# Kernel tuning notes

Measured on AMD Instinct MI355X. Metric: run time of the kernel, lower is better.

The kernel has to match this reference:

```python
import jax, jax.numpy as jnp
import numpy as np
from jax import lax

B, CIN, COUT, H, W, K = 256, 512, 256, 8, 8, 8192


def setup_inputs() -> dict:
    key = jax.random.key(0)
    ks = jax.random.split(key, 6)
    scale = 0.05
    return {
        "latent": jax.random.normal(ks[0], (B, CIN, H, W), dtype=jnp.float32),
        "conv_w": jax.random.normal(ks[1], (COUT, CIN, 3, 3), dtype=jnp.float32) * scale,
        "conv_b": jax.random.normal(ks[2], (COUT,), dtype=jnp.float32) * scale,
        "lin_w": jax.random.normal(ks[3], (COUT, COUT), dtype=jnp.float32) * scale,
        "lin_b": jax.random.normal(ks[4], (COUT,), dtype=jnp.float32) * scale,
        "emb": jax.random.normal(ks[5], (K, COUT), dtype=jnp.float32),
    }


def reference(latent, conv_w, conv_b, lin_w, lin_b, emb):
    # pre-quantization conv: 3x3, stride 1, padding 1 (SAME), NCHW / OIHW
    x = lax.conv_general_dilated(
        latent, conv_w, window_strides=(1, 1), padding="SAME",
        dimension_numbers=("NCHW", "OIHW", "NCHW"),
    ) + conv_b[None, :, None, None]
    # permute(0,2,3,1) then linear on last dim
    x = jnp.transpose(x, (0, 2, 3, 1))              # [B,H,W,C]
    x = jnp.einsum("bhwc,dc->bhwd", x, lin_w) + lin_b
    flat = x.reshape(-1, x.shape[-1])               # [B*H*W, C]
    distances = (
        jnp.sum(flat ** 2, axis=1, keepdims=True)
        + jnp.sum(emb ** 2, axis=1)
        - 2.0 * flat @ emb.T
    )                                               # [B*H*W, K]
    encoding_indices = jnp.argmin(distances, axis=1)
    return encoding_indices.reshape(-1, 64)
```

## Files before the change

kernel.cpp:

```cpp
#include <hip/hip_runtime.h>
#include <cstdint>
#include <cstddef>


#define CIN_  512
#define E_    4608
#define M_    16384

typedef _Float16 half4_t __attribute__((ext_vector_type(4)));
typedef _Float16 half8_t __attribute__((ext_vector_type(8)));
typedef float f32x4 __attribute__((ext_vector_type(4)));

#define GLOAD_LDS16(gptr, lptr)                                         \
    __builtin_amdgcn_global_load_lds(                                   \
        (const __attribute__((address_space(1))) unsigned int*)(gptr),  \
        (__attribute__((address_space(3))) unsigned int*)(lptr), 16, 0, 0)

__global__ void tkern(const float* __restrict__ src, float* __restrict__ dst,
                      int R, int C) {
    __shared__ float t[32][33];
    int c = blockIdx.x * 32 + threadIdx.x;
    int r = blockIdx.y * 32 + threadIdx.y;
    if (r < R && c < C) t[threadIdx.y][threadIdx.x] = src[(size_t)r * C + c];
    __syncthreads();
    int rr = blockIdx.x * 32 + threadIdx.y;
    int cc = blockIdx.y * 32 + threadIdx.x;
    if (rr < C && cc < R) dst[(size_t)rr * R + cc] = t[threadIdx.x][threadIdx.y];
}

__global__ __launch_bounds__(256) void fold5_k(const float* __restrict__ conv_w,
                                               const float* __restrict__ lwT,
                                               _Float16* __restrict__ W2x) {
    int e0 = blockIdx.x * 8;
    int d = threadIdx.x;
    float acc[8];
    #pragma unroll
    for (int j = 0; j < 8; ++j) acc[j] = 0.f;
    for (int co = 0; co < 256; ++co) {
        float lw = lwT[co * 256 + d];
        const float* cwr = conv_w + (size_t)co * E_ + e0;
        #pragma unroll
        for (int j = 0; j < 8; ++j) acc[j] += cwr[j] * lw;
    }
    #pragma unroll
    for (int j = 0; j < 8; ++j) {
        int e = e0 + j;
        int c = e / 9, t9 = e - c * 9;
        _Float16 h = (_Float16)acc[j];
        _Float16 l = (_Float16)(acc[j] - (float)h);
        W2x[((size_t)(t9 * 256 + d)) * 512 + c] = h;
        W2x[((size_t)((9 + t9) * 256 + d)) * 512 + c] = l;
    }
}

__global__ void bias_k(const float* __restrict__ lwT, const float* __restrict__ conv_b,
                       const float* __restrict__ lin_b, float* __restrict__ b2) {
    int d = threadIdx.x;
    float acc = lin_b[d];
    for (int co = 0; co < 256; ++co) acc += lwT[co * 256 + d] * conv_b[co];
    b2[d] = acc;
}

__global__ void embsq2_k(const float* __restrict__ emb, float* __restrict__ esq) {
    int w = threadIdx.x >> 6, lane = threadIdx.x & 63;
    #pragma unroll
    for (int it = 0; it < 4; ++it) {
        int k = (blockIdx.x + it * 512) * 4 + w;
        const float* row = emb + (size_t)k * 256;
        float s = 0.f;
        #pragma unroll
        for (int i = 0; i < 4; ++i) { float v = row[lane + 64 * i]; s += v * v; }
        #pragma unroll
        for (int m = 32; m >= 1; m >>= 1) s += __shfl_xor(s, m, 64);
        if (lane == 0) esq[k] = s;
    }
}

__global__ __launch_bounds__(256) void packlat_k(const float* __restrict__ lat,
                                                 _Float16* __restrict__ Xnp) {
    int b = blockIdx.x, t = threadIdx.x;
    __shared__ float lt[128][65];
    const float* src = lat + (size_t)b * 512 * 64;
    _Float16* dst = Xnp + (size_t)b * 64 * 1024;
    for (int c0 = 0; c0 < 512; c0 += 128) {
        __syncthreads();
        #pragma unroll
        for (int j = 0; j < 8; ++j) {
            int f4 = t + j * 256;
            int cc = f4 >> 4, p4 = (f4 & 15) * 4;
            float4 v = *(const float4*)(src + (size_t)(c0 + cc) * 64 + p4);
            lt[cc][p4] = v.x; lt[cc][p4 + 1] = v.y;
            lt[cc][p4 + 2] = v.z; lt[cc][p4 + 3] = v.w;
        }
        __syncthreads();
        int pix = t >> 2, cr = (t & 3) * 32;
        #pragma unroll
        for (int q = 0; q < 4; ++q) {
            half8_t hh, ll;
            #pragma unroll
            for (int j = 0; j < 8; ++j) {
                float v = lt[cr + q * 8 + j][pix];
                _Float16 h = (_Float16)v;
                hh[j] = h; ll[j] = (_Float16)(v - (float)h);
            }
            *(half8_t*)(dst + (size_t)pix * 1024 + c0 + cr + q * 8) = hh;
            *(half8_t*)(dst + (size_t)pix * 1024 + 512 + c0 + cr + q * 8) = ll;
        }
    }
}

__global__ __launch_bounds__(256) void convm4_k(
    const _Float16* __restrict__ Xnp, const _Float16* __restrict__ W2x,
    const float* __restrict__ b2, const _Float16* __restrict__ zp,
    float* __restrict__ yb) {
    __shared__ char sm[65536];
    int m0 = blockIdx.x * 128, n0 = blockIdx.y * 128;
    int tid = threadIdx.x, w = tid >> 6, lane = tid & 63;
    int wm = w & 1, wn = w >> 1;
    int fr = lane & 15, fq = lane >> 4;

    int xq = (fq ^ ((fr >> 1) & 3)) << 4;
    int aoff[4], boff[4];
    #pragma unroll
    for (int i = 0; i < 4; ++i) {
        aoff[i] = (wm * 64 + i * 16 + fr) * 64 + xq;
        boff[i] = (wn * 64 + i * 16 + fr) * 64 + xq;
    }
    int slt[2], sr[2], sq[2];
    #pragma unroll
    for (int i = 0; i < 2; ++i) {
        int s = w * 128 + i * 64 + lane;
        slt[i] = s;
        sr[i] = s >> 2;
        sq[i] = ((s & 3) ^ ((s >> 3) & 3)) * 8;
    }

    f32x4 acc[4][4];
    #pragma unroll
    for (int s = 0; s < 4; ++s)
        #pragma unroll
        for (int t = 0; t < 4; ++t)
            #pragma unroll
            for (int r = 0; r < 4; ++r) acc[s][t][r] = 0.f;

    auto stage = [&](int it, int buf) {
        int tap = it >> 4, cc = it & 15;
        int dy = tap / 3 - 1, dx = tap - (tap / 3) * 3 - 1;
        char* L = sm + buf * 32768;
        #pragma unroll
        for (int i = 0; i < 2; ++i) {
            int choff = cc * 32 + sq[i];
            int gm = m0 + sr[i];
            int img = gm >> 6, pix = gm & 63;
            int ih = (pix >> 3) + dy, iw = (pix & 7) + dx;
            bool v = ((unsigned)ih < 8u) && ((unsigned)iw < 8u);
            const _Float16* a0 = v
                ? Xnp + ((size_t)(img * 64 + ih * 8 + iw)) * 1024 : zp;
            const _Float16* a1 = v ? a0 + 512 : zp;
            GLOAD_LDS16(a0 + choff, L + slt[i] * 16);
            GLOAD_LDS16(a1 + choff, L + 8192 + slt[i] * 16);
            const _Float16* bb =
                W2x + ((size_t)(tap * 256 + n0 + sr[i])) * 512 + choff;
            GLOAD_LDS16(bb, L + 16384 + slt[i] * 16);
            GLOAD_LDS16(bb + (size_t)9 * 256 * 512, L + 24576 + slt[i] * 16);
        }
    };

    stage(0, 0);
    for (int it = 0; it < 144; ++it) {
        __syncthreads();
        if (it + 1 < 144) stage(it + 1, (it + 1) & 1);
        const char* L = sm + (it & 1) * 32768;
        half8_t ah[4], al[4], bh[4], bl[4];
        #pragma unroll
        for (int s = 0; s < 4; ++s) ah[s] = *(const half8_t*)(L + aoff[s]);
        #pragma unroll
        for (int t = 0; t < 4; ++t) bh[t] = *(const half8_t*)(L + 16384 + boff[t]);
        #pragma unroll
        for (int s = 0; s < 4; ++s)
            #pragma unroll
            for (int t = 0; t < 4; ++t)
                acc[s][t] = __builtin_amdgcn_mfma_f32_16x16x32_f16(
                    ah[s], bh[t], acc[s][t], 0, 0, 0);
        #pragma unroll
        for (int t = 0; t < 4; ++t) bl[t] = *(const half8_t*)(L + 24576 + boff[t]);
        #pragma unroll
        for (int s = 0; s < 4; ++s)
            #pragma unroll
            for (int t = 0; t < 4; ++t)
                acc[s][t] = __builtin_amdgcn_mfma_f32_16x16x32_f16(
                    ah[s], bl[t], acc[s][t], 0, 0, 0);
        #pragma unroll
        for (int s = 0; s < 4; ++s) al[s] = *(const half8_t*)(L + 8192 + aoff[s]);
        #pragma unroll
        for (int s = 0; s < 4; ++s)
            #pragma unroll
            for (int t = 0; t < 4; ++t)
                acc[s][t] = __builtin_amdgcn_mfma_f32_16x16x32_f16(
                    al[s], bh[t], acc[s][t], 0, 0, 0);
    }

    float bv[4];
    #pragma unroll
    for (int t = 0; t < 4; ++t) bv[t] = b2[n0 + wn * 64 + t * 16 + fr];
    #pragma unroll
    for (int s = 0; s < 4; ++s)
        #pragma unroll
        for (int r = 0; r < 4; ++r) {
            int m = m0 + wm * 64 + s * 16 + fq * 4 + r;
            #pragma unroll
            for (int t = 0; t < 4; ++t) {
                int d = n0 + wn * 64 + t * 16 + fr;
                yb[(size_t)m * 256 + d] = acc[s][t][r] + bv[t];
            }
        }
}

__global__ void packhi_s(const float* __restrict__ x, _Float16* __restrict__ o,
                         int iters) {
    for (int it = 0; it < iters; ++it) {
        int i = (blockIdx.x + it * 512) * 256 + threadIdx.x;
        float4 v = *(const float4*)(x + (size_t)i * 4);
        half4_t h = {(_Float16)v.x, (_Float16)v.y, (_Float16)v.z, (_Float16)v.w};
        *(half4_t*)(o + (size_t)i * 4) = h;
    }
}

__global__ __launch_bounds__(256) void screen6_k(
    const _Float16* __restrict__ A2, const _Float16* __restrict__ B2,
    const float* __restrict__ esq, float* __restrict__ ps2, int* __restrict__ pi2) {
    __shared__ char sm[32768];
    int m0 = blockIdx.x * 128, n0 = blockIdx.y * 128;
    int tid = threadIdx.x, w = tid >> 6, lane = tid & 63;
    int wm = w & 1, wn = w >> 1;
    int fr = lane & 15, fq = lane >> 4;

    int xq = (fq ^ ((fr >> 1) & 3)) << 4;
    int aoff[4], boff[4];
    #pragma unroll
    for (int i = 0; i < 4; ++i) {
        aoff[i] = (wm * 64 + i * 16 + fr) * 64 + xq;
        boff[i] = (wn * 64 + i * 16 + fr) * 64 + xq;
    }
    int slt[2], sr[2], sq[2];
    #pragma unroll
    for (int i = 0; i < 2; ++i) {
        int s = w * 128 + i * 64 + lane;
        slt[i] = s;
        sr[i] = s >> 2;
        sq[i] = ((s & 3) ^ ((s >> 3) & 3)) * 8;
    }

    auto stage = [&](int kt, int buf) {
        char* L = sm + buf * 16384;
        int ko = kt * 32;
        #pragma unroll
        for (int i = 0; i < 2; ++i) {
            GLOAD_LDS16(A2 + (size_t)(m0 + sr[i]) * 256 + ko + sq[i],
                        L + slt[i] * 16);
            GLOAD_LDS16(B2 + (size_t)(n0 + sr[i]) * 256 + ko + sq[i],
                        L + 8192 + slt[i] * 16);
        }
    };

    f32x4 acc[4][4];
    #pragma unroll
    for (int s = 0; s < 4; ++s)
        #pragma unroll
        for (int t = 0; t < 4; ++t)
            #pragma unroll
            for (int r = 0; r < 4; ++r) acc[s][t][r] = 0.f;

    stage(0, 0);
    for (int kt = 0; kt < 8; ++kt) {
        __syncthreads();
        if (kt + 1 < 8) stage(kt + 1, (kt + 1) & 1);
        const char* L = sm + (kt & 1) * 16384;
        half8_t af[4], bf[4];
        #pragma unroll
        for (int s = 0; s < 4; ++s) af[s] = *(const half8_t*)(L + aoff[s]);
        #pragma unroll
        for (int t = 0; t < 4; ++t) bf[t] = *(const half8_t*)(L + 8192 + boff[t]);
        #pragma unroll
        for (int s = 0; s < 4; ++s)
            #pragma unroll
            for (int t = 0; t < 4; ++t)
                acc[s][t] = __builtin_amdgcn_mfma_f32_16x16x32_f16(
                    af[s], bf[t], acc[s][t], 0, 0, 0);
    }

    float esv[4];
    #pragma unroll
    for (int t = 0; t < 4; ++t) esv[t] = esq[n0 + wn * 64 + t * 16 + fr];
    int colIdx = blockIdx.y * 2 + wn;
    #pragma unroll
    for (int s = 0; s < 4; ++s) {
        #pragma unroll
        for (int r = 0; r < 4; ++r) {
            float best = 3.4e38f; int bidx = 0x7fffffff;
            #pragma unroll
            for (int t = 0; t < 4; ++t) {
                float sc = esv[t] - 2.f * acc[s][t][r];
                int k = n0 + wn * 64 + t * 16 + fr;
                if (sc < best || (sc == best && k < bidx)) { best = sc; bidx = k; }
            }
            #pragma unroll
            for (int msk = 1; msk <= 8; msk <<= 1) {
                float so = __shfl_xor(best, msk, 64);
                int ko2 = __shfl_xor(bidx, msk, 64);
                if (so < best || (so == best && ko2 < bidx)) { best = so; bidx = ko2; }
            }
            if (fr == 0) {
                int m = m0 + wm * 64 + s * 16 + fq * 4 + r;
                ps2[(size_t)m * 128 + colIdx] = best;
                pi2[(size_t)m * 128 + colIdx] = bidx;
            }
        }
    }
}

__global__ __launch_bounds__(256) void refine3_k(
    const float* __restrict__ y, const float* __restrict__ emb,
    const float* __restrict__ esq, const float* __restrict__ ps2,
    const int* __restrict__ pi2, int* __restrict__ out) {
    int lane = threadIdx.x & 63;
    for (int j = 0; j < 8; ++j) {
        int m = blockIdx.x * 32 + j * 4 + (threadIdx.x >> 6);
        float4 yv = *(const float4*)(y + (size_t)m * 256 + lane * 4);
        float sc_[2]; int kc_[2];
        #pragma unroll
        for (int i = 0; i < 2; ++i) {
            sc_[i] = ps2[(size_t)m * 128 + lane * 2 + i];
            kc_[i] = pi2[(size_t)m * 128 + lane * 2 + i];
        }
        float s0 = fminf(sc_[0], sc_[1]);
        #pragma unroll
        for (int msk = 1; msk <= 32; msk <<= 1) s0 = fminf(s0, __shfl_xor(s0, msk, 64));
        float thr = s0 + 0.25f;
        float best = 3.4e38f; int bk = 0x7fffffff;
        for (int c = 0; c < 128; ++c) {
            float scc = __shfl(sc_[c & 1], c >> 1, 64);
            if (scc <= thr) {
                int k = __shfl(kc_[c & 1], c >> 1, 64);
                float4 ev = *(const float4*)(emb + (size_t)k * 256 + lane * 4);
                float d = yv.x * ev.x + yv.y * ev.y + yv.z * ev.z + yv.w * ev.w;
                #pragma unroll
                for (int msk = 1; msk <= 32; msk <<= 1) d += __shfl_xor(d, msk, 64);
                float sx = esq[k] - 2.f * d;
                if (sx < best || (sx == best && k < bk)) { best = sx; bk = k; }
            }
        }
        if (lane == 0) out[m] = bk;
    }
}

extern "C" void kernel_launch(void* const* d_in, const int* in_sizes, int n_in,
                              void* d_out, int out_size, void* d_ws, size_t ws_size,
                              hipStream_t stream) {
    const float* latent = (const float*)d_in[0];
    const float* conv_w = (const float*)d_in[1];
    const float* conv_b = (const float*)d_in[2];
    const float* lin_w  = (const float*)d_in[3];
    const float* lin_b  = (const float*)d_in[4];
    const float* emb    = (const float*)d_in[5];
    int* out = (int*)d_out;

    char* W = (char*)d_ws;
    float*    lwT = (float*)(W + 0);
    float*    b2  = (float*)(W + 262144);
    float*    esq = (float*)(W + 263168);
    float*    yb  = (float*)(W + 295936);
    _Float16* W2x = (_Float16*)(W + 17073152);
    _Float16* zp  = (_Float16*)(W + 21791744);
    _Float16* Xnp = (_Float16*)(W + 21792768);
    _Float16* A2  = (_Float16*)(W + 21792768);
    _Float16* B2  = (_Float16*)(W + 30181376);
    float*    ps2 = (float*)(W + 34375680);
    int*      pi2 = (int*)(W + 42764288);

    dim3 t32(32, 32);
    tkern<<<dim3(8, 8), t32, 0, stream>>>(lin_w, lwT, 256, 256);
    bias_k<<<1, 256, 0, stream>>>(lwT, conv_b, lin_b, b2);
    embsq2_k<<<512, 256, 0, stream>>>(emb, esq);
    fold5_k<<<576, 256, 0, stream>>>(conv_w, lwT, W2x);
    hipMemsetAsync(zp, 0, 1024, stream);
    packlat_k<<<256, 256, 0, stream>>>(latent, Xnp);

    convm4_k<<<dim3(128, 2), 256, 0, stream>>>(Xnp, W2x, b2, zp, yb);

    packhi_s<<<512, 256, 0, stream>>>(yb, A2, 8);
    packhi_s<<<512, 256, 0, stream>>>(emb, B2, 4);
    screen6_k<<<dim3(128, 64), 256, 0, stream>>>(A2, B2, esq, ps2, pi2);
    refine3_k<<<512, 256, 0, stream>>>(yb, emb, esq, ps2, pi2, out);
}
```

Baseline: 505.7 us.

## Reuse A tile across conv taps, fuse pack kernels, XCD-aware screen tile mapping

The conv kernel now loads each 128-pixel channel slice of the latent into LDS once per channel chunk and reuses it across all 9 taps. Each tap's shift is applied through the LDS read address with zeroed fragments at borders, so A-side global traffic drops about ninefold and the zero-pad buffer and memset go away. The two fp16 pack launches and the embedding-norm kernel are merged into one kernel. The screen kernel remaps a 1D grid so that blocks sharing M tiles land on the same XCD, which should improve L2 reuse. The cost is more LDS address arithmetic and selects inside the inner loop.

```diff
diff --git a/kernel.cpp b/kernel.cpp
--- a/kernel.cpp
+++ b/kernel.cpp
@@ -61,21 +61,6 @@
     b2[d] = acc;
 }
 
-__global__ void embsq2_k(const float* __restrict__ emb, float* __restrict__ esq) {
-    int w = threadIdx.x >> 6, lane = threadIdx.x & 63;
-    #pragma unroll
-    for (int it = 0; it < 4; ++it) {
-        int k = (blockIdx.x + it * 512) * 4 + w;
-        const float* row = emb + (size_t)k * 256;
-        float s = 0.f;
-        #pragma unroll
-        for (int i = 0; i < 4; ++i) { float v = row[lane + 64 * i]; s += v * v; }
-        #pragma unroll
-        for (int m = 32; m >= 1; m >>= 1) s += __shfl_xor(s, m, 64);
-        if (lane == 0) esq[k] = s;
-    }
-}
-
 __global__ __launch_bounds__(256) void packlat_k(const float* __restrict__ lat,
                                                  _Float16* __restrict__ Xnp) {
     int b = blockIdx.x, t = threadIdx.x;
@@ -109,10 +94,9 @@
     }
 }
 
-__global__ __launch_bounds__(256) void convm4_k(
+__global__ __launch_bounds__(256) void convm6_k(
     const _Float16* __restrict__ Xnp, const _Float16* __restrict__ W2x,
-    const float* __restrict__ b2, const _Float16* __restrict__ zp,
-    float* __restrict__ yb) {
+    const float* __restrict__ b2, float* __restrict__ yb) {
     __shared__ char sm[65536];
     int m0 = blockIdx.x * 128, n0 = blockIdx.y * 128;
     int tid = threadIdx.x, w = tid >> 6, lane = tid & 63;
@@ -120,11 +104,14 @@
     int fr = lane & 15, fq = lane >> 4;
 
     int xq = (fq ^ ((fr >> 1) & 3)) << 4;
-    int aoff[4], boff[4];
-    #pragma unroll
-    for (int i = 0; i < 4; ++i) {
-        aoff[i] = (wm * 64 + i * 16 + fr) * 64 + xq;
-        boff[i] = (wn * 64 + i * 16 + fr) * 64 + xq;
+    int boff[4];
+    #pragma unroll
+    for (int i = 0; i < 4; ++i) boff[i] = (wn * 64 + i * 16 + fr) * 64 + xq;
+    int imgoff[4], ph[4], pw[4];
+    #pragma unroll
+    for (int s = 0; s < 4; ++s) {
+        int rr = wm * 64 + s * 16 + fr;
+        imgoff[s] = rr & 64; ph[s] = (rr >> 3) & 7; pw[s] = rr & 7;
     }
     int slt[2], sr[2], sq[2];
     #pragma unroll
@@ -135,6 +122,27 @@
         sq[i] = ((s & 3) ^ ((s >> 3) & 3)) * 8;
     }
 
+    auto stageA = [&](int cc, int buf) {
+        char* L = sm + buf * 16384;
+        #pragma unroll
+        for (int i = 0; i < 2; ++i) {
+            const _Float16* base =
+                Xnp + (size_t)(m0 + sr[i]) * 1024 + cc * 32 + sq[i];
+            GLOAD_LDS16(base, L + slt[i] * 16);
+            GLOAD_LDS16(base + 512, L + 8192 + slt[i] * 16);
+        }
+    };
+    auto stageB = [&](int tap, int cc, int buf) {
+        char* L = sm + 32768 + buf * 16384;
+        #pragma unroll
+        for (int i = 0; i < 2; ++i) {
+            const _Float16* bb =
+                W2x + ((size_t)(tap * 256 + n0 + sr[i])) * 512 + cc * 32 + sq[i];
+            GLOAD_LDS16(bb, L + slt[i] * 16);
+            GLOAD_LDS16(bb + (size_t)9 * 256 * 512, L + 8192 + slt[i] * 16);
+        }
+    };
+
     f32x4 acc[4][4];
     #pragma unroll
     for (int s = 0; s < 4; ++s)
@@ -143,61 +151,57 @@
             #pragma unroll
             for (int r = 0; r < 4; ++r) acc[s][t][r] = 0.f;
 
-    auto stage = [&](int it, int buf) {
-        int tap = it >> 4, cc = it & 15;
-        int dy = tap / 3 - 1, dx = tap - (tap / 3) * 3 - 1;
-        char* L = sm + buf * 32768;
-        #pragma unroll
-        for (int i = 0; i < 2; ++i) {
-            int choff = cc * 32 + sq[i];
-            int gm = m0 + sr[i];
-            int img = gm >> 6, pix = gm & 63;
-            int ih = (pix >> 3) + dy, iw = (pix & 7) + dx;
-            bool v = ((unsigned)ih < 8u) && ((unsigned)iw < 8u);
-            const _Float16* a0 = v
-                ? Xnp + ((size_t)(img * 64 + ih * 8 + iw)) * 1024 : zp;
-            const _Float16* a1 = v ? a0 + 512 : zp;
-            GLOAD_LDS16(a0 + choff, L + slt[i] * 16);
-            GLOAD_LDS16(a1 + choff, L + 8192 + slt[i] * 16);
-            const _Float16* bb =
-                W2x + ((size_t)(tap * 256 + n0 + sr[i])) * 512 + choff;
-            GLOAD_LDS16(bb, L + 16384 + slt[i] * 16);
-            GLOAD_LDS16(bb + (size_t)9 * 256 * 512, L + 24576 + slt[i] * 16);
-        }
-    };
-
-    stage(0, 0);
-    for (int it = 0; it < 144; ++it) {
-        __syncthreads();
-        if (it + 1 < 144) stage(it + 1, (it + 1) & 1);
-        const char* L = sm + (it & 1) * 32768;
-        half8_t ah[4], al[4], bh[4], bl[4];
-        #pragma unroll
-        for (int s = 0; s < 4; ++s) ah[s] = *(const half8_t*)(L + aoff[s]);
-        #pragma unroll
-        for (int t = 0; t < 4; ++t) bh[t] = *(const half8_t*)(L + 16384 + boff[t]);
-        #pragma unroll
-        for (int s = 0; s < 4; ++s)
-            #pragma unroll
-            for (int t = 0; t < 4; ++t)
-                acc[s][t] = __builtin_amdgcn_mfma_f32_16x16x32_f16(
-                    ah[s], bh[t], acc[s][t], 0, 0, 0);
-        #pragma unroll
-        for (int t = 0; t < 4; ++t) bl[t] = *(const half8_t*)(L + 24576 + boff[t]);
-        #pragma unroll
-        for (int s = 0; s < 4; ++s)
-            #pragma unroll
-            for (int t = 0; t < 4; ++t)
-                acc[s][t] = __builtin_amdgcn_mfma_f32_16x16x32_f16(
-                    ah[s], bl[t], acc[s][t], 0, 0, 0);
-        #pragma unroll
-        for (int s = 0; s < 4; ++s) al[s] = *(const half8_t*)(L + 8192 + aoff[s]);
-        #pragma unroll
-        for (int s = 0; s < 4; ++s)
-            #pragma unroll
-            for (int t = 0; t < 4; ++t)
-                acc[s][t] = __builtin_amdgcn_mfma_f32_16x16x32_f16(
-                    al[s], bh[t], acc[s][t], 0, 0, 0);
+    stageA(0, 0);
+    stageB(0, 0, 0);
+    const half8_t zfrag = {};
+    int gi = 0;
+    for (int cc = 0; cc < 16; ++cc) {
+        const char* Ab = sm + (cc & 1) * 16384;
+        for (int tap = 0; tap < 9; ++tap, ++gi) {
+            __syncthreads();
+            if (tap < 8) stageB(tap + 1, cc, (gi + 1) & 1);
+            else if (cc < 15) stageB(0, cc + 1, (gi + 1) & 1);
+            if (tap == 7 && cc < 15) stageA(cc + 1, (cc + 1) & 1);
+
+            int dy = tap / 3 - 1, dx = tap - (tap / 3) * 3 - 1;
+            half8_t ah[4], al[4];
+            #pragma unroll
+            for (int s = 0; s < 4; ++s) {
+                int ih = ph[s] + dy, iw = pw[s] + dx;
+                bool v = ((unsigned)ih < 8u) && ((unsigned)iw < 8u);
+                int pp = imgoff[s] + (v ? ih * 8 + iw : 0);
+                int ao = pp * 64 + ((fq ^ ((pp >> 1) & 3)) << 4);
+                half8_t a0 = *(const half8_t*)(Ab + ao);
+                half8_t a1 = *(const half8_t*)(Ab + 8192 + ao);
+                ah[s] = v ? a0 : zfrag;
+                al[s] = v ? a1 : zfrag;
+            }
+            const char* Bb = sm + 32768 + (gi & 1) * 16384;
+            half8_t bh[4], bl[4];
+            #pragma unroll
+            for (int t = 0; t < 4; ++t) {
+                bh[t] = *(const half8_t*)(Bb + boff[t]);
+                bl[t] = *(const half8_t*)(Bb + 8192 + boff[t]);
+            }
+            #pragma unroll
+            for (int s = 0; s < 4; ++s)
+                #pragma unroll
+                for (int t = 0; t < 4; ++t)
+                    acc[s][t] = __builtin_amdgcn_mfma_f32_16x16x32_f16(
+                        ah[s], bh[t], acc[s][t], 0, 0, 0);
+            #pragma unroll
+            for (int s = 0; s < 4; ++s)
+                #pragma unroll
+                for (int t = 0; t < 4; ++t)
+                    acc[s][t] = __builtin_amdgcn_mfma_f32_16x16x32_f16(
+                        ah[s], bl[t], acc[s][t], 0, 0, 0);
+            #pragma unroll
+            for (int s = 0; s < 4; ++s)
+                #pragma unroll
+                for (int t = 0; t < 4; ++t)
+                    acc[s][t] = __builtin_amdgcn_mfma_f32_16x16x32_f16(
+                        al[s], bh[t], acc[s][t], 0, 0, 0);
+        }
     }
 
     float bv[4];
@@ -216,21 +220,40 @@
         }
 }
 
-__global__ void packhi_s(const float* __restrict__ x, _Float16* __restrict__ o,
-                         int iters) {
-    for (int it = 0; it < iters; ++it) {
+__global__ __launch_bounds__(256) void pack2_k(
+    const float* __restrict__ yb, const float* __restrict__ emb,
+    _Float16* __restrict__ A2, _Float16* __restrict__ B2,
+    float* __restrict__ esq) {
+    #pragma unroll
+    for (int it = 0; it < 8; ++it) {
         int i = (blockIdx.x + it * 512) * 256 + threadIdx.x;
-        float4 v = *(const float4*)(x + (size_t)i * 4);
+        float4 v = *(const float4*)(yb + (size_t)i * 4);
         half4_t h = {(_Float16)v.x, (_Float16)v.y, (_Float16)v.z, (_Float16)v.w};
-        *(half4_t*)(o + (size_t)i * 4) = h;
-    }
-}
-
-__global__ __launch_bounds__(256) void screen6_k(
+        *(half4_t*)(A2 + (size_t)i * 4) = h;
+    }
+    int w = threadIdx.x >> 6, lane = threadIdx.x & 63;
+    #pragma unroll
+    for (int j = 0; j < 4; ++j) {
+        int k = blockIdx.x * 16 + w * 4 + j;
+        float4 v = *(const float4*)(emb + (size_t)k * 256 + lane * 4);
+        half4_t h = {(_Float16)v.x, (_Float16)v.y, (_Float16)v.z, (_Float16)v.w};
+        *(half4_t*)(B2 + (size_t)k * 256 + lane * 4) = h;
+        float s = v.x * v.x + v.y * v.y + v.z * v.z + v.w * v.w;
+        #pragma unroll
+        for (int m = 32; m >= 1; m >>= 1) s += __shfl_xor(s, m, 64);
+        if (lane == 0) esq[k] = s;
+    }
+}
+
+__global__ __launch_bounds__(256) void screen7_k(
     const _Float16* __restrict__ A2, const _Float16* __restrict__ B2,
     const float* __restrict__ esq, float* __restrict__ ps2, int* __restrict__ pi2) {
     __shared__ char sm[32768];
-    int m0 = blockIdx.x * 128, n0 = blockIdx.y * 128;
+    int Lb = blockIdx.x;
+    int xcd = Lb & 7, j = Lb >> 3;
+    int mt = xcd * 16 + (j & 15);
+    int nt = j >> 4;
+    int m0 = mt * 128, n0 = nt * 128;
     int tid = threadIdx.x, w = tid >> 6, lane = tid & 63;
     int wm = w & 1, wn = w >> 1;
     int fr = lane & 15, fq = lane >> 4;
@@ -292,7 +315,7 @@
     float esv[4];
     #pragma unroll
     for (int t = 0; t < 4; ++t) esv[t] = esq[n0 + wn * 64 + t * 16 + fr];
-    int colIdx = blockIdx.y * 2 + wn;
+    int colIdx = nt * 2 + wn;
     #pragma unroll
     for (int s = 0; s < 4; ++s) {
         #pragma unroll
@@ -371,7 +394,6 @@
     float*    esq = (float*)(W + 263168);
     float*    yb  = (float*)(W + 295936);
     _Float16* W2x = (_Float16*)(W + 17073152);
-    _Float16* zp  = (_Float16*)(W + 21791744);
     _Float16* Xnp = (_Float16*)(W + 21792768);
     _Float16* A2  = (_Float16*)(W + 21792768);
     _Float16* B2  = (_Float16*)(W + 30181376);
@@ -381,15 +403,12 @@
     dim3 t32(32, 32);
     tkern<<<dim3(8, 8), t32, 0, stream>>>(lin_w, lwT, 256, 256);
     bias_k<<<1, 256, 0, stream>>>(lwT, conv_b, lin_b, b2);
-    embsq2_k<<<512, 256, 0, stream>>>(emb, esq);
     fold5_k<<<576, 256, 0, stream>>>(conv_w, lwT, W2x);
-    hipMemsetAsync(zp, 0, 1024, stream);
     packlat_k<<<256, 256, 0, stream>>>(latent, Xnp);
 
-    convm4_k<<<dim3(128, 2), 256, 0, stream>>>(Xnp, W2x, b2, zp, yb);
-
-    packhi_s<<<512, 256, 0, stream>>>(yb, A2, 8);
-    packhi_s<<<512, 256, 0, stream>>>(emb, B2, 4);
-    screen6_k<<<dim3(128, 64), 256, 0, stream>>>(A2, B2, esq, ps2, pi2);
+    convm6_k<<<dim3(128, 2), 256, 0, stream>>>(Xnp, W2x, b2, yb);
+
+    pack2_k<<<512, 256, 0, stream>>>(yb, emb, A2, B2, esq);
+    screen7_k<<<8192, 256, 0, stream>>>(A2, B2, esq, ps2, pi2);
     refine3_k<<<512, 256, 0, stream>>>(yb, emb, esq, ps2, pi2, out);
 }
```

Result: faster. 473.8 us (-6.3%).
